# Optimization experiments

Measured on AMD Instinct MI355X. Metric: run time of the kernel, lower is better.

The kernel has to match this reference:

```python
import jax, jax.numpy as jnp
import numpy as np

B, T, D = 8, 4096, 512
MAX_SEG = 32  # max_segment_len


def setup_inputs() -> dict:
    key = jax.random.key(0)
    ks = jax.random.split(key, 8)
    s = 0.02
    return {
        "x": jax.random.normal(ks[0], (B, T, D), dtype=jnp.float32),
        "W1": jax.random.normal(ks[1], (D // 2, D), dtype=jnp.float32) * s,
        "b1": jnp.zeros((D // 2,), jnp.float32),
        "W2": jax.random.normal(ks[2], (2, D // 2), dtype=jnp.float32) * s,
        "b2": jnp.zeros((2,), jnp.float32),
        "W_ih": jax.random.normal(ks[3], (4 * D, D), dtype=jnp.float32) * s,
        "W_hh": jax.random.normal(ks[4], (4 * D, D), dtype=jnp.float32) * s,
        "b_ih": jax.random.normal(ks[5], (4 * D,), dtype=jnp.float32) * s,
        "b_hh": jax.random.normal(ks[6], (4 * D,), dtype=jnp.float32) * s,
    }


def reference(x, W1, b1, W2, b2, W_ih, W_hh, b_ih, b_hh):
    Bb, Tt, Dd = x.shape

    # boundary predictor (eval mode: dropout = identity, erf-based GELU)
    h1 = jax.nn.gelu(jnp.einsum('btd,hd->bth', x, W1) + b1, approximate=False)
    boundary_logits = jnp.einsum('bth,gh->btg', h1, W2) + b2  # [B,T,2]
    probs = jax.nn.softmax(boundary_logits, axis=-1)
    bnd = (probs[..., 1] > 0.5).astype(jnp.float32)

    # forced boundaries every MAX_SEG steps and at T-1
    forced = np.arange(MAX_SEG, Tt, MAX_SEG)
    bnd = bnd.at[:, forced].set(1.0).at[:, Tt - 1].set(1.0)
    is_b = bnd > 0.5                                     # [B,T] bool

    # a segment starts at t if t==0 or there was a boundary at t-1
    reset = jnp.concatenate([jnp.ones((Bb, 1), bool), is_b[:, :-1]], axis=1)

    # segmented LSTM scan: state resets at segment starts; hidden at a boundary
    # position t equals the LSTM final hidden over segment [start..t]
    gates_x = jnp.einsum('btd,gd->btg', x, W_ih) + b_ih + b_hh  # [B,T,4D]

    def scan_one(gx, rs):
        def step(carry, inp):
            h, c = carry
            g, r = inp
            h = jnp.where(r, 0.0, h)
            c = jnp.where(r, 0.0, c)
            g = g + W_hh @ h
            i, f, gg, o = jnp.split(g, 4)  # torch gate order i,f,g,o
            c = jax.nn.sigmoid(f) * c + jax.nn.sigmoid(i) * jnp.tanh(gg)
            h = jax.nn.sigmoid(o) * jnp.tanh(c)
            return (h, c), h
        z = jnp.zeros((Dd,), gx.dtype)
        _, hs = jax.lax.scan(step, (z, z), (gx, rs))
        return hs

    hs = jax.vmap(scan_one)(gates_x, reset)  # [B,T,D]

    # a segment is emitted at t iff boundary at t and segment length >= 2
    # (i.e. t is not itself a segment start)
    emit = is_b & ~reset                      # [B,T]
    seg_idx = jnp.cumsum(emit.astype(jnp.int32), axis=1) - 1
    dest = jnp.where(emit, seg_idx, Tt)       # non-emitted rows dumped at col T
    barr = jnp.arange(Bb)[:, None]

    padded = jnp.zeros((Bb, Tt + 1, Dd), x.dtype)
    padded = padded.at[barr, dest].set(hs)[:, :Tt]       # [B,T,D], zero padded

    bidx = jnp.full((Bb, Tt + 1), -1, jnp.int32)
    tgrid = jnp.broadcast_to(jnp.arange(Tt, dtype=jnp.int32)[None, :], (Bb, Tt))
    bidx = bidx.at[barr, dest].set(tgrid)[:, :Tt]        # [B,T], -1 padded

    # fallback when no segment was emitted: mean over time, boundary index T-1
    counts = emit.sum(axis=1)
    fb = counts == 0
    padded = padded.at[:, 0].set(jnp.where(fb[:, None], x.mean(axis=1), padded[:, 0]))
    bidx = bidx.at[:, 0].set(jnp.where(fb, Tt - 1, bidx[:, 0]))

    return padded, bidx, boundary_logits
```

## Files before the change

kernel.cpp:

```cpp
#include <hip/hip_runtime.h>
#include <math.h>

#define B 8
#define T 4096
#define D 512
#define H1 256
#define R 1024
#define BIDX_OFF ((size_t)B*T*D)
#define LOG_OFF  ((size_t)B*T*D + B*T)

typedef __attribute__((ext_vector_type(8))) short short8;
typedef __attribute__((ext_vector_type(4))) float f32x4;

__device__ inline unsigned short f2bf_hi(float f) {
  unsigned u = __float_as_uint(f);
  u += 0x7FFF + ((u >> 16) & 1);
  return (unsigned short)(u >> 16);
}
__device__ inline float bf2f(unsigned short b) {
  return __uint_as_float(((unsigned)b) << 16);
}
__device__ inline float sigm(float v) { return 1.f / (1.f + expf(-v)); }

__global__ __launch_bounds__(256) void k_prep(const float* __restrict__ x,
                                              const float* __restrict__ Wih,
                                              const float* __restrict__ Whh,
                                              const float* __restrict__ bih,
                                              const float* __restrict__ bhh,
                                              const float* __restrict__ W1,
                                              float* __restrict__ out,
                                              unsigned short* __restrict__ xhi,
                                              unsigned short* __restrict__ WhhH,
                                              unsigned short* __restrict__ WhhL,
                                              unsigned short* __restrict__ WxH,
                                              float* __restrict__ bsum,
                                              unsigned short* __restrict__ W1t0,
                                              unsigned short* __restrict__ W1t1,
                                              unsigned short* __restrict__ W1t2) {
  int gid = blockIdx.x * 256 + threadIdx.x;
  float4 z4 = make_float4(0.f, 0.f, 0.f, 0.f);
  float4* o4 = (float4*)out;
#pragma unroll
  for (int i = 0; i < 4; ++i) o4[(size_t)i * 1048576 + gid] = z4;
  {
    const float* xs = x + (size_t)gid * 16;
    unsigned short hv[16];
#pragma unroll
    for (int q = 0; q < 4; ++q) {
      float4 v = *(const float4*)(xs + q * 4);
      hv[q * 4 + 0] = f2bf_hi(v.x); hv[q * 4 + 1] = f2bf_hi(v.y);
      hv[q * 4 + 2] = f2bf_hi(v.z); hv[q * 4 + 3] = f2bf_hi(v.w);
    }
    uint4 p0, p1;
    p0.x = (unsigned)hv[0] | ((unsigned)hv[1] << 16);  p0.y = (unsigned)hv[2] | ((unsigned)hv[3] << 16);
    p0.z = (unsigned)hv[4] | ((unsigned)hv[5] << 16);  p0.w = (unsigned)hv[6] | ((unsigned)hv[7] << 16);
    p1.x = (unsigned)hv[8] | ((unsigned)hv[9] << 16);  p1.y = (unsigned)hv[10] | ((unsigned)hv[11] << 16);
    p1.z = (unsigned)hv[12] | ((unsigned)hv[13] << 16); p1.w = (unsigned)hv[14] | ((unsigned)hv[15] << 16);
    *(uint4*)(xhi + (size_t)gid * 16) = p0;
    *(uint4*)(xhi + (size_t)gid * 16 + 8) = p1;
  }
  {
    int n = gid >> 9, k = gid & 511;
    int d = n >> 2, g = n & 3;
    size_t oo = (size_t)(g * 512 + d) * 512 + k;
    float wx = Wih[oo], wh = Whh[oo];
    WxH[(size_t)n * 512 + k] = f2bf_hi(wx);
    unsigned short hh = f2bf_hi(wh);
    WhhH[(size_t)n * 512 + k] = hh;
    WhhL[(size_t)n * 512 + k] = f2bf_hi(wh - bf2f(hh));
    if (k == 0) bsum[n] = bih[g * 512 + d] + bhh[g * 512 + d];
  }
  if (gid < 16384) {
    int base = gid * 8;
    float4 a = *(const float4*)(W1 + base);
    float4 b = *(const float4*)(W1 + base + 4);
    float fv[8] = {a.x, a.y, a.z, a.w, b.x, b.y, b.z, b.w};
    unsigned short t0[8], t1[8], t2[8];
#pragma unroll
    for (int j = 0; j < 8; ++j) {
      unsigned short h0 = f2bf_hi(fv[j]);
      float r1 = fv[j] - bf2f(h0);
      unsigned short h1v = f2bf_hi(r1);
      float r2 = r1 - bf2f(h1v);
      t0[j] = h0; t1[j] = h1v; t2[j] = f2bf_hi(r2);
    }
    uint4 p0, p1, p2;
    p0.x = (unsigned)t0[0] | ((unsigned)t0[1] << 16); p0.y = (unsigned)t0[2] | ((unsigned)t0[3] << 16);
    p0.z = (unsigned)t0[4] | ((unsigned)t0[5] << 16); p0.w = (unsigned)t0[6] | ((unsigned)t0[7] << 16);
    p1.x = (unsigned)t1[0] | ((unsigned)t1[1] << 16); p1.y = (unsigned)t1[2] | ((unsigned)t1[3] << 16);
    p1.z = (unsigned)t1[4] | ((unsigned)t1[5] << 16); p1.w = (unsigned)t1[6] | ((unsigned)t1[7] << 16);
    p2.x = (unsigned)t2[0] | ((unsigned)t2[1] << 16); p2.y = (unsigned)t2[2] | ((unsigned)t2[3] << 16);
    p2.z = (unsigned)t2[4] | ((unsigned)t2[5] << 16); p2.w = (unsigned)t2[6] | ((unsigned)t2[7] << 16);
    *(uint4*)(W1t0 + base) = p0;
    *(uint4*)(W1t1 + base) = p1;
    *(uint4*)(W1t2 + base) = p2;
  }
}

__global__ __launch_bounds__(256) void k_bnd1f(const float* __restrict__ x,
                                               const unsigned short* __restrict__ T0,
                                               const unsigned short* __restrict__ T1,
                                               const unsigned short* __restrict__ T2,
                                               const float* __restrict__ b1,
                                               const float* __restrict__ W2,
                                               const float* __restrict__ b2,
                                               float* __restrict__ out,
                                               unsigned char* __restrict__ flags) {
  __shared__ unsigned short A0[64][40], A1[64][40], A2[64][40];
  __shared__ float part[2][64][2];
  __shared__ float lsm[64][2];
  int row0 = blockIdx.x * 64;
  int tid = threadIdx.x;
  int arow = tid >> 2, ak0 = (tid & 3) * 8;
  const float* xrow = x + (size_t)(row0 + arow) * 512;
  int w = tid >> 6, l = tid & 63;
  int wm = w >> 1, wn = w & 1;
  int lrow = l & 15, lk = (l >> 4) * 8;

  f32x4 acc[2][8];
#pragma unroll
  for (int i = 0; i < 2; ++i)
#pragma unroll
    for (int j = 0; j < 8; ++j) acc[i][j] = (f32x4)(0.f);

  for (int kb = 0; kb < 512; kb += 32) {
    float4 a0v = *(const float4*)(xrow + kb + ak0);
    float4 a1v = *(const float4*)(xrow + kb + ak0 + 4);
    float fv[8] = {a0v.x, a0v.y, a0v.z, a0v.w, a1v.x, a1v.y, a1v.z, a1v.w};
    unsigned short s0[8], s1[8], s2[8];
#pragma unroll
    for (int j = 0; j < 8; ++j) {
      unsigned short h0 = f2bf_hi(fv[j]);
      float r1 = fv[j] - bf2f(h0);
      unsigned short h1v = f2bf_hi(r1);
      float r2 = r1 - bf2f(h1v);
      s0[j] = h0; s1[j] = h1v; s2[j] = f2bf_hi(r2);
    }
    uint4 p;
    p.x = (unsigned)s0[0] | ((unsigned)s0[1] << 16); p.y = (unsigned)s0[2] | ((unsigned)s0[3] << 16);
    p.z = (unsigned)s0[4] | ((unsigned)s0[5] << 16); p.w = (unsigned)s0[6] | ((unsigned)s0[7] << 16);
    *(uint4*)&A0[arow][ak0] = p;
    p.x = (unsigned)s1[0] | ((unsigned)s1[1] << 16); p.y = (unsigned)s1[2] | ((unsigned)s1[3] << 16);
    p.z = (unsigned)s1[4] | ((unsigned)s1[5] << 16); p.w = (unsigned)s1[6] | ((unsigned)s1[7] << 16);
    *(uint4*)&A1[arow][ak0] = p;
    p.x = (unsigned)s2[0] | ((unsigned)s2[1] << 16); p.y = (unsigned)s2[2] | ((unsigned)s2[3] << 16);
    p.z = (unsigned)s2[4] | ((unsigned)s2[5] << 16); p.w = (unsigned)s2[6] | ((unsigned)s2[7] << 16);
    *(uint4*)&A2[arow][ak0] = p;
    __syncthreads();

    short8 a0f[2], a1f[2], a2f[2];
#pragma unroll
    for (int fi = 0; fi < 2; ++fi) {
      a0f[fi] = *(const short8*)&A0[wm * 32 + fi * 16 + lrow][lk];
      a1f[fi] = *(const short8*)&A1[wm * 32 + fi * 16 + lrow][lk];
      a2f[fi] = *(const short8*)&A2[wm * 32 + fi * 16 + lrow][lk];
    }
#pragma unroll
    for (int fj = 0; fj < 8; ++fj) {
      size_t bo = (size_t)(wn * 128 + fj * 16 + lrow) * 512 + kb + lk;
      short8 b0 = *(const short8*)(T0 + bo);
      short8 b1v = *(const short8*)(T1 + bo);
      short8 b2v = *(const short8*)(T2 + bo);
#pragma unroll
      for (int fi = 0; fi < 2; ++fi) {
        acc[fi][fj] = __builtin_amdgcn_mfma_f32_16x16x32_bf16(a0f[fi], b0, acc[fi][fj], 0, 0, 0);
        acc[fi][fj] = __builtin_amdgcn_mfma_f32_16x16x32_bf16(a0f[fi], b1v, acc[fi][fj], 0, 0, 0);
        acc[fi][fj] = __builtin_amdgcn_mfma_f32_16x16x32_bf16(a1f[fi], b0, acc[fi][fj], 0, 0, 0);
        acc[fi][fj] = __builtin_amdgcn_mfma_f32_16x16x32_bf16(a1f[fi], b1v, acc[fi][fj], 0, 0, 0);
        acc[fi][fj] = __builtin_amdgcn_mfma_f32_16x16x32_bf16(a0f[fi], b2v, acc[fi][fj], 0, 0, 0);
        acc[fi][fj] = __builtin_amdgcn_mfma_f32_16x16x32_bf16(a2f[fi], b0, acc[fi][fj], 0, 0, 0);
      }
    }
    __syncthreads();
  }

  float b1v[8], w20[8], w21[8];
#pragma unroll
  for (int fj = 0; fj < 8; ++fj) {
    int col = wn * 128 + fj * 16 + lrow;
    b1v[fj] = b1[col];
    w20[fj] = W2[col];
    w21[fj] = W2[H1 + col];
  }
  float p0[2][4], p1[2][4];
#pragma unroll
  for (int fi = 0; fi < 2; ++fi)
#pragma unroll
    for (int reg = 0; reg < 4; ++reg) { p0[fi][reg] = 0.f; p1[fi][reg] = 0.f; }
#pragma unroll
  for (int fi = 0; fi < 2; ++fi)
#pragma unroll
    for (int fj = 0; fj < 8; ++fj)
#pragma unroll
      for (int reg = 0; reg < 4; ++reg) {
        float v = acc[fi][fj][reg] + b1v[fj];
        float ge = 0.5f * v * (1.0f + erff(v * 0.70710678118654752f));
        p0[fi][reg] = fmaf(ge, w20[fj], p0[fi][reg]);
        p1[fi][reg] = fmaf(ge, w21[fj], p1[fi][reg]);
      }
#pragma unroll
  for (int off = 1; off < 16; off <<= 1)
#pragma unroll
    for (int fi = 0; fi < 2; ++fi)
#pragma unroll
      for (int reg = 0; reg < 4; ++reg) {
        p0[fi][reg] += __shfl_xor(p0[fi][reg], off);
        p1[fi][reg] += __shfl_xor(p1[fi][reg], off);
      }
  if (lrow == 0) {
    int hi = l >> 4;
#pragma unroll
    for (int fi = 0; fi < 2; ++fi)
#pragma unroll
      for (int reg = 0; reg < 4; ++reg) {
        int rloc = wm * 32 + fi * 16 + hi * 4 + reg;
        part[wn][rloc][0] = p0[fi][reg];
        part[wn][rloc][1] = p1[fi][reg];
      }
  }
  __syncthreads();
  if (tid < 128) {
    int r = tid >> 1, g = tid & 1;
    float lg = part[0][r][g] + part[1][r][g] + b2[g];
    int rowg = row0 + r;
    out[LOG_OFF + (size_t)rowg * 2 + g] = lg;
    lsm[r][g] = lg;
  }
  __syncthreads();
  if (tid < 64) {
    int rowg = row0 + tid;
    int t = rowg & (T - 1);
    bool forced = (((t & 31) == 0) && t != 0) || (t == T - 1);
    flags[rowg] = (forced || (lsm[tid][1] > lsm[tid][0])) ? 1 : 0;
  }
}

__global__ __launch_bounds__(256) void k_seg(unsigned char* __restrict__ flags,
                                             int* __restrict__ segidx,
                                             int* __restrict__ counts,
                                             float* __restrict__ out) {
  int b = blockIdx.x, tid = threadIdx.x;
  __shared__ int sc[256];
  const int PER = T / 256;
  int base = tid * PER;
  bool em[PER];
  unsigned char prev = (tid == 0) ? 0 : (unsigned char)(flags[b * T + base - 1] & 1);
  int cnt = 0;
  for (int i = 0; i < PER; ++i) {
    int t = base + i;
    unsigned char cur = flags[b * T + t] & 1;
    bool reset = (t == 0) || (prev != 0);
    bool e = (cur != 0) && !reset;
    em[i] = e;
    cnt += e ? 1 : 0;
    flags[b * T + t] = (unsigned char)(cur | (reset ? 2 : 0) | (e ? 4 : 0));
    prev = cur;
  }
  sc[tid] = cnt;
  __syncthreads();
  for (int off = 1; off < 256; off <<= 1) {
    int v = (tid >= off) ? sc[tid - off] : 0;
    __syncthreads();
    sc[tid] += v;
    __syncthreads();
  }
  int total = sc[255];
  int run = sc[tid] - cnt;
  for (int i = 0; i < PER; ++i) {
    if (em[i]) { segidx[b * T + base + i] = run; run++; }
  }
  for (int j = tid; j < T; j += 256) out[BIDX_OFF + (size_t)b * T + j] = -1.0f;
  __syncthreads();
  run = sc[tid] - cnt;
  for (int i = 0; i < PER; ++i) {
    if (em[i]) { out[BIDX_OFF + (size_t)b * T + run] = (float)(base + i); run++; }
  }
  if (tid == 0) counts[b] = total;
}

__global__ __launch_bounds__(256) void k_gx(const unsigned short* __restrict__ xhi,
                                            const unsigned short* __restrict__ WxH,
                                            unsigned short* __restrict__ gx) {
  __shared__ unsigned short As[128][40], Bs[128][40];
  __shared__ unsigned short Cs[64][136];
  int m0 = blockIdx.x * 128, n0 = blockIdx.y * 128;
  int tid = threadIdx.x;
  int row = tid >> 1, col0 = (tid & 1) * 16;
  const unsigned short* asrc = xhi + (size_t)(m0 + row) * 512 + col0;
  const unsigned short* bsrc = WxH + (size_t)(n0 + row) * 512 + col0;

  int w = tid >> 6, l = tid & 63;
  int wm = w >> 1, wn = w & 1;
  int lrow = l & 15, lk = (l >> 4) * 8;

  f32x4 acc[4][4];
#pragma unroll
  for (int i = 0; i < 4; ++i)
#pragma unroll
    for (int j = 0; j < 4; ++j) acc[i][j] = (f32x4)(0.f);

  uint4 rA0 = *(const uint4*)asrc,       rA1 = *(const uint4*)(asrc + 8);
  uint4 rB0 = *(const uint4*)bsrc,       rB1 = *(const uint4*)(bsrc + 8);

  for (int it = 0; it < 16; ++it) {
    *(uint4*)&As[row][col0] = rA0;  *(uint4*)&As[row][col0 + 8] = rA1;
    *(uint4*)&Bs[row][col0] = rB0;  *(uint4*)&Bs[row][col0 + 8] = rB1;
    __syncthreads();
    if (it < 15) {
      int ko = (it + 1) * 32;
      rA0 = *(const uint4*)(asrc + ko);  rA1 = *(const uint4*)(asrc + ko + 8);
      rB0 = *(const uint4*)(bsrc + ko);  rB1 = *(const uint4*)(bsrc + ko + 8);
    }
    short8 af[4], bf[4];
#pragma unroll
    for (int fi = 0; fi < 4; ++fi) {
      af[fi] = *(const short8*)&As[wm * 64 + fi * 16 + lrow][lk];
      bf[fi] = *(const short8*)&Bs[wn * 64 + fi * 16 + lrow][lk];
    }
#pragma unroll
    for (int fi = 0; fi < 4; ++fi)
#pragma unroll
      for (int fj = 0; fj < 4; ++fj)
        acc[fi][fj] = __builtin_amdgcn_mfma_f32_16x16x32_bf16(af[fi], bf[fj], acc[fi][fj], 0, 0, 0);
    __syncthreads();
  }

#pragma unroll
  for (int h = 0; h < 2; ++h) {
    if (wm == h) {
#pragma unroll
      for (int fi = 0; fi < 4; ++fi)
#pragma unroll
        for (int fj = 0; fj < 4; ++fj) {
          int lr = fi * 16 + (l >> 4) * 4;
          int lc = wn * 64 + fj * 16 + lrow;
#pragma unroll
          for (int reg = 0; reg < 4; ++reg)
            Cs[lr + reg][lc] = f2bf_hi(acc[fi][fj][reg]);
        }
    }
    __syncthreads();
    int crow = tid >> 2, c0 = (tid & 3) * 32;
    size_t gbase = (size_t)(m0 + h * 64 + crow) * 2048 + n0 + c0;
    *(uint4*)(gx + gbase)      = *(uint4*)&Cs[crow][c0];
    *(uint4*)(gx + gbase + 8)  = *(uint4*)&Cs[crow][c0 + 8];
    *(uint4*)(gx + gbase + 16) = *(uint4*)&Cs[crow][c0 + 16];
    *(uint4*)(gx + gbase + 24) = *(uint4*)&Cs[crow][c0 + 24];
    __syncthreads();
  }
}

__global__ __launch_bounds__(256) void k_cell0(const unsigned short* __restrict__ gx,
                                               const float* __restrict__ bsum,
                                               const unsigned char* __restrict__ flags,
                                               const int* __restrict__ segidx,
                                               unsigned short* __restrict__ Hhi,
                                               unsigned short* __restrict__ Hlo,
                                               float* __restrict__ Cb,
                                               float* __restrict__ out) {
  int id = blockIdx.x * 256 + threadIdx.x;
  int rr = id >> 9, d = id & 511;
  int ch = rr & 127, bb = rr >> 7;
  int t = ch ? (32 * ch + 1) : 0;
  uint2 gp = *(const uint2*)(gx + ((size_t)(bb * T + t) * 2048 + 4 * d));
  float4 bsv = *(const float4*)&bsum[4 * d];
  float gi_ = bf2f((unsigned short)(gp.x & 0xffff)) + bsv.x;
  float gz_ = bf2f((unsigned short)(gp.y & 0xffff)) + bsv.z;
  float go_ = bf2f((unsigned short)(gp.y >> 16)) + bsv.w;
  float c = sigm(gi_) * tanhf(gz_);
  float h = sigm(go_) * tanhf(c);
  unsigned char fl = flags[bb * T + t];
  if (fl & 4) {
    int si = segidx[bb * T + t];
    out[(size_t)(bb * T + si) * D + d] = h;
  }
  bool isb = (fl & 1) != 0;
  float he = isb ? 0.f : h;
  float ce = isb ? 0.f : c;
  Cb[(size_t)rr * D + d] = ce;
  unsigned short hh = f2bf_hi(he);
  Hhi[(size_t)rr * D + d] = hh;
  Hlo[(size_t)rr * D + d] = f2bf_hi(he - bf2f(hh));
}

__global__ __launch_bounds__(256) void k_step2(const unsigned short* __restrict__ gx,
                                               const unsigned short* __restrict__ WhhH,
                                               const unsigned short* __restrict__ WhhL,
                                               const unsigned short* __restrict__ HhR,
                                               const unsigned short* __restrict__ HlR,
                                               unsigned short* __restrict__ HhW,
                                               unsigned short* __restrict__ HlW,
                                               float* __restrict__ Cb,
                                               const float* __restrict__ bsum,
                                               const unsigned char* __restrict__ flags,
                                               const int* __restrict__ segidx,
                                               float* __restrict__ out, int s) {
  __shared__ unsigned short Ah[64][72], Al[64][72], Bh[64][72], Bl[64][72];
  __shared__ float Ct[64][68];
  int id = blockIdx.x;
  int swz = (id & 7) * 64 + (id >> 3);
  int bn = swz >> 4, bm = swz & 15;
  int tid = threadIdx.x;
  int row = tid >> 2, col0 = (tid & 3) * 16;
  int ra = bm * 64 + row;
  const unsigned short* ah_src = HhR + (size_t)ra * D;
  const unsigned short* al_src = HlR + (size_t)ra * D;
  const unsigned short* bh_src = WhhH + (size_t)(bn * 64 + row) * D;
  const unsigned short* bl_src = WhhL + (size_t)(bn * 64 + row) * D;

  int w = tid >> 6, l = tid & 63;
  int wm = w >> 1, wn = w & 1;
  int lrow = l & 15, lk = (l >> 4) * 8;

  f32x4 acc[2][2];
#pragma unroll
  for (int i = 0; i < 2; ++i)
#pragma unroll
    for (int j = 0; j < 2; ++j) acc[i][j] = (f32x4)(0.f);

  uint4 rAh0 = *(const uint4*)(ah_src + col0), rAh1 = *(const uint4*)(ah_src + col0 + 8);
  uint4 rAl0 = *(const uint4*)(al_src + col0), rAl1 = *(const uint4*)(al_src + col0 + 8);
  uint4 rBh0 = *(const uint4*)(bh_src + col0), rBh1 = *(const uint4*)(bh_src + col0 + 8);
  uint4 rBl0 = *(const uint4*)(bl_src + col0), rBl1 = *(const uint4*)(bl_src + col0 + 8);

  for (int kk = 0; kk < 8; ++kk) {
    *(uint4*)&Ah[row][col0] = rAh0;  *(uint4*)&Ah[row][col0 + 8] = rAh1;
    *(uint4*)&Al[row][col0] = rAl0;  *(uint4*)&Al[row][col0 + 8] = rAl1;
    *(uint4*)&Bh[row][col0] = rBh0;  *(uint4*)&Bh[row][col0 + 8] = rBh1;
    *(uint4*)&Bl[row][col0] = rBl0;  *(uint4*)&Bl[row][col0 + 8] = rBl1;
    __syncthreads();
    if (kk < 7) {
      int ko = (kk + 1) * 64 + col0;
      rAh0 = *(const uint4*)(ah_src + ko); rAh1 = *(const uint4*)(ah_src + ko + 8);
      rAl0 = *(const uint4*)(al_src + ko); rAl1 = *(const uint4*)(al_src + ko + 8);
      rBh0 = *(const uint4*)(bh_src + ko); rBh1 = *(const uint4*)(bh_src + ko + 8);
      rBl0 = *(const uint4*)(bl_src + ko); rBl1 = *(const uint4*)(bl_src + ko + 8);
    }
#pragma unroll
    for (int ks = 0; ks < 2; ++ks) {
      short8 ah0 = *(const short8*)&Ah[wm * 32 + lrow][ks * 32 + lk];
      short8 ah1 = *(const short8*)&Ah[wm * 32 + 16 + lrow][ks * 32 + lk];
      short8 al0 = *(const short8*)&Al[wm * 32 + lrow][ks * 32 + lk];
      short8 al1 = *(const short8*)&Al[wm * 32 + 16 + lrow][ks * 32 + lk];
      short8 bh0 = *(const short8*)&Bh[wn * 32 + lrow][ks * 32 + lk];
      short8 bh1 = *(const short8*)&Bh[wn * 32 + 16 + lrow][ks * 32 + lk];
      short8 bl0 = *(const short8*)&Bl[wn * 32 + lrow][ks * 32 + lk];
      short8 bl1 = *(const short8*)&Bl[wn * 32 + 16 + lrow][ks * 32 + lk];
      acc[0][0] = __builtin_amdgcn_mfma_f32_16x16x32_bf16(ah0, bh0, acc[0][0], 0, 0, 0);
      acc[0][1] = __builtin_amdgcn_mfma_f32_16x16x32_bf16(ah0, bh1, acc[0][1], 0, 0, 0);
      acc[1][0] = __builtin_amdgcn_mfma_f32_16x16x32_bf16(ah1, bh0, acc[1][0], 0, 0, 0);
      acc[1][1] = __builtin_amdgcn_mfma_f32_16x16x32_bf16(ah1, bh1, acc[1][1], 0, 0, 0);
      acc[0][0] = __builtin_amdgcn_mfma_f32_16x16x32_bf16(ah0, bl0, acc[0][0], 0, 0, 0);
      acc[0][1] = __builtin_amdgcn_mfma_f32_16x16x32_bf16(ah0, bl1, acc[0][1], 0, 0, 0);
      acc[1][0] = __builtin_amdgcn_mfma_f32_16x16x32_bf16(ah1, bl0, acc[1][0], 0, 0, 0);
      acc[1][1] = __builtin_amdgcn_mfma_f32_16x16x32_bf16(ah1, bl1, acc[1][1], 0, 0, 0);
      acc[0][0] = __builtin_amdgcn_mfma_f32_16x16x32_bf16(al0, bh0, acc[0][0], 0, 0, 0);
      acc[0][1] = __builtin_amdgcn_mfma_f32_16x16x32_bf16(al0, bh1, acc[0][1], 0, 0, 0);
      acc[1][0] = __builtin_amdgcn_mfma_f32_16x16x32_bf16(al1, bh0, acc[1][0], 0, 0, 0);
      acc[1][1] = __builtin_amdgcn_mfma_f32_16x16x32_bf16(al1, bh1, acc[1][1], 0, 0, 0);
    }
    __syncthreads();
  }

#pragma unroll
  for (int fi = 0; fi < 2; ++fi)
#pragma unroll
    for (int fj = 0; fj < 2; ++fj) {
      int crow = wm * 32 + fi * 16 + (l >> 4) * 4;
      int ccol = wn * 32 + fj * 16 + lrow;
#pragma unroll
      for (int reg = 0; reg < 4; ++reg)
        Ct[crow + reg][ccol] = acc[fi][fj][reg];
    }
  __syncthreads();

  int d_loc = tid & 15, rb = tid >> 4;
  int d_g = bn * 16 + d_loc;
  float4 bsv = *(const float4*)&bsum[(size_t)4 * d_g];
#pragma unroll
  for (int j = 0; j < 4; ++j) {
    int r_loc = rb + 16 * j;
    int r = bm * 64 + r_loc;
    int ch = r & 127, bb = r >> 7;
    int len = (ch == 0) ? 33 : ((ch == 127) ? 31 : 32);
    if (s >= len) continue;
    int t = (ch ? (32 * ch + 1) : 0) + s;
    unsigned char fl = flags[bb * T + t];
    float4 g = *(float4*)&Ct[r_loc][4 * d_loc];
    uint2 gp = *(const uint2*)(gx + ((size_t)(bb * T + t) * 2048 + 4 * d_g));
    float gi = g.x + bsv.x + bf2f((unsigned short)(gp.x & 0xffff));
    float gf = g.y + bsv.y + bf2f((unsigned short)(gp.x >> 16));
    float gz = g.z + bsv.z + bf2f((unsigned short)(gp.y & 0xffff));
    float go = g.w + bsv.w + bf2f((unsigned short)(gp.y >> 16));
    float cp = Cb[(size_t)r * D + d_g];
    float c = sigm(gf) * cp + sigm(gi) * tanhf(gz);
    float h = sigm(go) * tanhf(c);
    if (fl & 4) {
      int si = segidx[bb * T + t];
      out[(size_t)(bb * T + si) * D + d_g] = h;
    }
    bool isb = (fl & 1) != 0;
    float he = isb ? 0.f : h;
    float ce = isb ? 0.f : c;
    Cb[(size_t)r * D + d_g] = ce;
    unsigned short hh = f2bf_hi(he);
    HhW[(size_t)r * D + d_g] = hh;
    HlW[(size_t)r * D + d_g] = f2bf_hi(he - bf2f(hh));
  }
}

__global__ __launch_bounds__(256) void k_tail(const unsigned short* __restrict__ gx,
                                              const unsigned short* __restrict__ WhhH,
                                              const unsigned short* __restrict__ WhhL,
                                              const unsigned short* __restrict__ Hhi,
                                              const unsigned short* __restrict__ Hlo,
                                              const float* __restrict__ Cb,
                                              const float* __restrict__ bsum,
                                              const unsigned char* __restrict__ flags,
                                              const int* __restrict__ segidx,
                                              float* __restrict__ out) {
  __shared__ float hsh[512];
  __shared__ float gsh[128][4];
  int bb = blockIdx.x >> 2, q = blockIdx.x & 3;
  int r = bb * 128;
  int tid = threadIdx.x;
  for (int i = tid; i < 512; i += 256)
    hsh[i] = bf2f(Hhi[(size_t)r * 512 + i]) + bf2f(Hlo[(size_t)r * 512 + i]);
  __syncthreads();
  int dd_loc = tid >> 1;
  int dd = q * 128 + dd_loc;
  int pair = tid & 1;
#pragma unroll
  for (int gg = 0; gg < 2; ++gg) {
    int n = 4 * dd + 2 * pair + gg;
    const unsigned short* wh = WhhH + (size_t)n * 512;
    const unsigned short* wl = WhhL + (size_t)n * 512;
    float sacc = 0.f;
    for (int k = 0; k < 512; k += 8) {
      uint4 ph = *(const uint4*)(wh + k);
      uint4 pl = *(const uint4*)(wl + k);
      unsigned pu[4] = {ph.x, ph.y, ph.z, ph.w};
      unsigned lu[4] = {pl.x, pl.y, pl.z, pl.w};
#pragma unroll
      for (int j = 0; j < 4; ++j) {
        float w0 = bf2f((unsigned short)(pu[j] & 0xffff)) + bf2f((unsigned short)(lu[j] & 0xffff));
        float w1 = bf2f((unsigned short)(pu[j] >> 16)) + bf2f((unsigned short)(lu[j] >> 16));
        sacc = fmaf(w0, hsh[k + 2 * j], sacc);
        sacc = fmaf(w1, hsh[k + 2 * j + 1], sacc);
      }
    }
    unsigned short gxv = gx[(size_t)(bb * T + 32) * 2048 + n];
    gsh[dd_loc][2 * pair + gg] = sacc + bf2f(gxv) + bsum[n];
  }
  __syncthreads();
  if (pair == 0) {
    unsigned char fl = flags[bb * T + 32];
    float gi = gsh[dd_loc][0], gf = gsh[dd_loc][1], gz = gsh[dd_loc][2], go = gsh[dd_loc][3];
    float cp = Cb[(size_t)r * 512 + dd];
    float c = sigm(gf) * cp + sigm(gi) * tanhf(gz);
    float h = sigm(go) * tanhf(c);
    if (fl & 4) {
      int si = segidx[bb * T + 32];
      out[(size_t)(bb * T + si) * D + dd] = h;
    }
  }
}

__global__ __launch_bounds__(256) void k_fb(const float* __restrict__ x,
                                            const int* __restrict__ counts,
                                            float* __restrict__ out) {
  int b = blockIdx.x;
  if (counts[b] != 0) return;
  int tid = threadIdx.x;
  for (int d = tid; d < D; d += 256) {
    float sum = 0.f;
    for (int t = 0; t < T; ++t) sum += x[(size_t)(b * T + t) * D + d];
    out[(size_t)(b * T) * D + d] = sum / (float)T;
  }
  if (tid == 0) out[BIDX_OFF + (size_t)b * T] = (float)(T - 1);
}


extern "C" void kernel_launch(void* const* d_in, const int* in_sizes, int n_in,
                              void* d_out, int out_size, void* d_ws, size_t ws_size,
                              hipStream_t stream) {
  const float* x   = (const float*)d_in[0];
  const float* W1  = (const float*)d_in[1];
  const float* b1  = (const float*)d_in[2];
  const float* W2  = (const float*)d_in[3];
  const float* b2  = (const float*)d_in[4];
  const float* Wih = (const float*)d_in[5];
  const float* Whh = (const float*)d_in[6];
  const float* bih = (const float*)d_in[7];
  const float* bhh = (const float*)d_in[8];
  float* out = (float*)d_out;
  char* ws = (char*)d_ws;
  const size_t MB = 1 << 20;

  unsigned char* flags = (unsigned char*)(ws + 0);
  int* counts = (int*)(ws + 32768);
  int* segidx = (int*)(ws + 65536);
  unsigned short* Hh0  = (unsigned short*)(ws + 1 * MB);
  unsigned short* Hl0  = (unsigned short*)(ws + 2 * MB);
  unsigned short* Hh1  = (unsigned short*)(ws + 3 * MB);
  unsigned short* Hl1  = (unsigned short*)(ws + 4 * MB);
  float* Cb            = (float*)(ws + 5 * MB);
  unsigned short* WhhH = (unsigned short*)(ws + 7 * MB);
  unsigned short* WhhL = (unsigned short*)(ws + 9 * MB);
  unsigned short* WxH  = (unsigned short*)(ws + 11 * MB);
  float* bsum          = (float*)(ws + 13 * MB);
  unsigned short* W1t0 = (unsigned short*)(ws + 13 * MB + 262144);
  unsigned short* W1t1 = (unsigned short*)(ws + 13 * MB + 2 * 262144);
  unsigned short* W1t2 = (unsigned short*)(ws + 13 * MB + 3 * 262144);
  unsigned short* xhi  = (unsigned short*)(ws + 14 * MB);
  unsigned short* gx   = (unsigned short*)(ws + 46 * MB);

  hipLaunchKernelGGL(k_prep, dim3(4096), dim3(256), 0, stream,
                     x, Wih, Whh, bih, bhh, W1, out, xhi, WhhH, WhhL, WxH,
                     bsum, W1t0, W1t1, W1t2);
  hipLaunchKernelGGL(k_bnd1f, dim3(512), dim3(256), 0, stream,
                     x, W1t0, W1t1, W1t2, b1, W2, b2, out, flags);
  hipLaunchKernelGGL(k_seg, dim3(8), dim3(256), 0, stream, flags, segidx, counts, out);
  hipLaunchKernelGGL(k_gx, dim3(256, 16), dim3(256), 0, stream, xhi, WxH, gx);
  hipLaunchKernelGGL(k_cell0, dim3(2048), dim3(256), 0, stream, gx, bsum, flags, segidx, Hh0, Hl0, Cb, out);
  for (int s = 1; s < 32; ++s) {
    const unsigned short* HhR = ((s - 1) & 1) ? Hh1 : Hh0;
    const unsigned short* HlR = ((s - 1) & 1) ? Hl1 : Hl0;
    unsigned short* HhW = (s & 1) ? Hh1 : Hh0;
    unsigned short* HlW = (s & 1) ? Hl1 : Hl0;
    hipLaunchKernelGGL(k_step2, dim3(512), dim3(256), 0, stream,
                       gx, WhhH, WhhL, HhR, HlR, HhW, HlW, Cb, bsum, flags, segidx, out, s);
  }
  hipLaunchKernelGGL(k_tail, dim3(32), dim3(256), 0, stream,
                     gx, WhhH, WhhL, Hh1, Hl1, Cb, bsum, flags, segidx, out);
  hipLaunchKernelGGL(k_fb, dim3(8), dim3(256), 0, stream, x, counts, out);
}
```

Measured before the change: 848.0 us.

## Split boundary MLP into tiled GEMM with LDS-staged weights plus logit kernel

```diff
diff --git a/kernel.cpp b/kernel.cpp
--- a/kernel.cpp
+++ b/kernel.cpp
@@ -97,31 +97,29 @@
   }
 }
 
-__global__ __launch_bounds__(256) void k_bnd1f(const float* __restrict__ x,
-                                               const unsigned short* __restrict__ T0,
-                                               const unsigned short* __restrict__ T1,
-                                               const unsigned short* __restrict__ T2,
-                                               const float* __restrict__ b1,
-                                               const float* __restrict__ W2,
-                                               const float* __restrict__ b2,
-                                               float* __restrict__ out,
-                                               unsigned char* __restrict__ flags) {
-  __shared__ unsigned short A0[64][40], A1[64][40], A2[64][40];
-  __shared__ float part[2][64][2];
-  __shared__ float lsm[64][2];
-  int row0 = blockIdx.x * 64;
+__global__ __launch_bounds__(256) void k_bnd1(const float* __restrict__ x,
+                                              const unsigned short* __restrict__ T0,
+                                              const unsigned short* __restrict__ T1,
+                                              const unsigned short* __restrict__ T2,
+                                              const float* __restrict__ b1,
+                                              float* __restrict__ h1out) {
+  __shared__ unsigned short A0[64][48], A1[64][48], A2[64][48];
+  __shared__ unsigned short B0[64][48], B1[64][48], B2[64][48];
+  int bm = blockIdx.x, bnn = blockIdx.y;
   int tid = threadIdx.x;
   int arow = tid >> 2, ak0 = (tid & 3) * 8;
-  const float* xrow = x + (size_t)(row0 + arow) * 512;
+  const float* xrow = x + (size_t)(bm * 64 + arow) * 512;
+  size_t wro = (size_t)(bnn * 64 + arow) * 512;
+
   int w = tid >> 6, l = tid & 63;
   int wm = w >> 1, wn = w & 1;
   int lrow = l & 15, lk = (l >> 4) * 8;
 
-  f32x4 acc[2][8];
+  f32x4 acc[2][2];
 #pragma unroll
   for (int i = 0; i < 2; ++i)
 #pragma unroll
-    for (int j = 0; j < 8; ++j) acc[i][j] = (f32x4)(0.f);
+    for (int j = 0; j < 2; ++j) acc[i][j] = (f32x4)(0.f);
 
   for (int kb = 0; kb < 512; kb += 32) {
     float4 a0v = *(const float4*)(xrow + kb + ak0);
@@ -146,92 +144,83 @@
     p.x = (unsigned)s2[0] | ((unsigned)s2[1] << 16); p.y = (unsigned)s2[2] | ((unsigned)s2[3] << 16);
     p.z = (unsigned)s2[4] | ((unsigned)s2[5] << 16); p.w = (unsigned)s2[6] | ((unsigned)s2[7] << 16);
     *(uint4*)&A2[arow][ak0] = p;
-    __syncthreads();
-
-    short8 a0f[2], a1f[2], a2f[2];
+
+    *(uint4*)&B0[arow][ak0] = *(const uint4*)(T0 + wro + kb + ak0);
+    *(uint4*)&B1[arow][ak0] = *(const uint4*)(T1 + wro + kb + ak0);
+    *(uint4*)&B2[arow][ak0] = *(const uint4*)(T2 + wro + kb + ak0);
+    __syncthreads();
+
+    short8 a0f[2], a1f[2], a2f[2], b0f[2], b1f[2], b2f[2];
 #pragma unroll
     for (int fi = 0; fi < 2; ++fi) {
       a0f[fi] = *(const short8*)&A0[wm * 32 + fi * 16 + lrow][lk];
       a1f[fi] = *(const short8*)&A1[wm * 32 + fi * 16 + lrow][lk];
       a2f[fi] = *(const short8*)&A2[wm * 32 + fi * 16 + lrow][lk];
-    }
-#pragma unroll
-    for (int fj = 0; fj < 8; ++fj) {
-      size_t bo = (size_t)(wn * 128 + fj * 16 + lrow) * 512 + kb + lk;
-      short8 b0 = *(const short8*)(T0 + bo);
-      short8 b1v = *(const short8*)(T1 + bo);
-      short8 b2v = *(const short8*)(T2 + bo);
-#pragma unroll
-      for (int fi = 0; fi < 2; ++fi) {
-        acc[fi][fj] = __builtin_amdgcn_mfma_f32_16x16x32_bf16(a0f[fi], b0, acc[fi][fj], 0, 0, 0);
-        acc[fi][fj] = __builtin_amdgcn_mfma_f32_16x16x32_bf16(a0f[fi], b1v, acc[fi][fj], 0, 0, 0);
-        acc[fi][fj] = __builtin_amdgcn_mfma_f32_16x16x32_bf16(a1f[fi], b0, acc[fi][fj], 0, 0, 0);
-        acc[fi][fj] = __builtin_amdgcn_mfma_f32_16x16x32_bf16(a1f[fi], b1v, acc[fi][fj], 0, 0, 0);
-        acc[fi][fj] = __builtin_amdgcn_mfma_f32_16x16x32_bf16(a0f[fi], b2v, acc[fi][fj], 0, 0, 0);
-        acc[fi][fj] = __builtin_amdgcn_mfma_f32_16x16x32_bf16(a2f[fi], b0, acc[fi][fj], 0, 0, 0);
+      b0f[fi] = *(const short8*)&B0[wn * 32 + fi * 16 + lrow][lk];
+      b1f[fi] = *(const short8*)&B1[wn * 32 + fi * 16 + lrow][lk];
+      b2f[fi] = *(const short8*)&B2[wn * 32 + fi * 16 + lrow][lk];
+    }
+#pragma unroll
+    for (int fi = 0; fi < 2; ++fi)
+#pragma unroll
+      for (int fj = 0; fj < 2; ++fj) {
+        acc[fi][fj] = __builtin_amdgcn_mfma_f32_16x16x32_bf16(a0f[fi], b0f[fj], acc[fi][fj], 0, 0, 0);
+        acc[fi][fj] = __builtin_amdgcn_mfma_f32_16x16x32_bf16(a0f[fi], b1f[fj], acc[fi][fj], 0, 0, 0);
+        acc[fi][fj] = __builtin_amdgcn_mfma_f32_16x16x32_bf16(a1f[fi], b0f[fj], acc[fi][fj], 0, 0, 0);
+        acc[fi][fj] = __builtin_amdgcn_mfma_f32_16x16x32_bf16(a1f[fi], b1f[fj], acc[fi][fj], 0, 0, 0);
+        acc[fi][fj] = __builtin_amdgcn_mfma_f32_16x16x32_bf16(a0f[fi], b2f[fj], acc[fi][fj], 0, 0, 0);
+        acc[fi][fj] = __builtin_amdgcn_mfma_f32_16x16x32_bf16(a2f[fi], b0f[fj], acc[fi][fj], 0, 0, 0);
       }
-    }
-    __syncthreads();
-  }
-
-  float b1v[8], w20[8], w21[8];
-#pragma unroll
-  for (int fj = 0; fj < 8; ++fj) {
-    int col = wn * 128 + fj * 16 + lrow;
-    b1v[fj] = b1[col];
-    w20[fj] = W2[col];
-    w21[fj] = W2[H1 + col];
-  }
-  float p0[2][4], p1[2][4];
+    __syncthreads();
+  }
 #pragma unroll
   for (int fi = 0; fi < 2; ++fi)
 #pragma unroll
-    for (int reg = 0; reg < 4; ++reg) { p0[fi][reg] = 0.f; p1[fi][reg] = 0.f; }
-#pragma unroll
-  for (int fi = 0; fi < 2; ++fi)
-#pragma unroll
-    for (int fj = 0; fj < 8; ++fj)
+    for (int fj = 0; fj < 2; ++fj) {
+      int rrow = bm * 64 + wm * 32 + fi * 16 + (l >> 4) * 4;
+      int rcol = bnn * 64 + wn * 32 + fj * 16 + lrow;
+      float bv = b1[rcol];
 #pragma unroll
       for (int reg = 0; reg < 4; ++reg) {
-        float v = acc[fi][fj][reg] + b1v[fj];
+        float v = acc[fi][fj][reg] + bv;
         float ge = 0.5f * v * (1.0f + erff(v * 0.70710678118654752f));
-        p0[fi][reg] = fmaf(ge, w20[fj], p0[fi][reg]);
-        p1[fi][reg] = fmaf(ge, w21[fj], p1[fi][reg]);
+        h1out[(size_t)(rrow + reg) * H1 + rcol] = ge;
       }
-#pragma unroll
-  for (int off = 1; off < 16; off <<= 1)
-#pragma unroll
-    for (int fi = 0; fi < 2; ++fi)
-#pragma unroll
-      for (int reg = 0; reg < 4; ++reg) {
-        p0[fi][reg] += __shfl_xor(p0[fi][reg], off);
-        p1[fi][reg] += __shfl_xor(p1[fi][reg], off);
-      }
-  if (lrow == 0) {
-    int hi = l >> 4;
-#pragma unroll
-    for (int fi = 0; fi < 2; ++fi)
-#pragma unroll
-      for (int reg = 0; reg < 4; ++reg) {
-        int rloc = wm * 32 + fi * 16 + hi * 4 + reg;
-        part[wn][rloc][0] = p0[fi][reg];
-        part[wn][rloc][1] = p1[fi][reg];
-      }
-  }
-  __syncthreads();
-  if (tid < 128) {
-    int r = tid >> 1, g = tid & 1;
-    float lg = part[0][r][g] + part[1][r][g] + b2[g];
-    int rowg = row0 + r;
-    out[LOG_OFF + (size_t)rowg * 2 + g] = lg;
-    lsm[r][g] = lg;
-  }
-  __syncthreads();
-  if (tid < 64) {
-    int rowg = row0 + tid;
-    int t = rowg & (T - 1);
+    }
+}
+
+__global__ __launch_bounds__(256) void k_log(const float* __restrict__ h1,
+                                             const float* __restrict__ W2,
+                                             const float* __restrict__ b2,
+                                             float* __restrict__ out,
+                                             unsigned char* __restrict__ flags) {
+  int tid = threadIdx.x;
+  int row = blockIdx.x * 32 + (tid >> 3);
+  int part = tid & 7;
+  const float* hr = h1 + (size_t)row * H1 + part * 32;
+  const float* w0 = W2 + part * 32;
+  const float* w1 = W2 + H1 + part * 32;
+  float s0 = 0.f, s1 = 0.f;
+#pragma unroll
+  for (int q = 0; q < 8; ++q) {
+    float4 hv = *(const float4*)(hr + q * 4);
+    float4 w0v = *(const float4*)(w0 + q * 4);
+    float4 w1v = *(const float4*)(w1 + q * 4);
+    s0 = fmaf(hv.x, w0v.x, fmaf(hv.y, w0v.y, fmaf(hv.z, w0v.z, fmaf(hv.w, w0v.w, s0))));
+    s1 = fmaf(hv.x, w1v.x, fmaf(hv.y, w1v.y, fmaf(hv.z, w1v.z, fmaf(hv.w, w1v.w, s1))));
+  }
+#pragma unroll
+  for (int off = 4; off >= 1; off >>= 1) {
+    s0 += __shfl_xor(s0, off);
+    s1 += __shfl_xor(s1, off);
+  }
+  if (part == 0) {
+    float l0 = s0 + b2[0], l1 = s1 + b2[1];
+    out[LOG_OFF + (size_t)row * 2]     = l0;
+    out[LOG_OFF + (size_t)row * 2 + 1] = l1;
+    int t = row & (T - 1);
     bool forced = (((t & 31) == 0) && t != 0) || (t == T - 1);
-    flags[rowg] = (forced || (lsm[tid][1] > lsm[tid][0])) ? 1 : 0;
+    flags[row] = (forced || (l1 > l0)) ? 1 : 0;
   }
 }
 
@@ -398,8 +387,8 @@
   __shared__ unsigned short Ah[64][72], Al[64][72], Bh[64][72], Bl[64][72];
   __shared__ float Ct[64][68];
   int id = blockIdx.x;
-  int swz = (id & 7) * 64 + (id >> 3);
-  int bn = swz >> 4, bm = swz & 15;
+  int bm = (id & 7) * 2 + (id >> 8);
+  int bn = (id >> 3) & 31;
   int tid = threadIdx.x;
   int row = tid >> 2, col0 = (tid & 3) * 16;
   int ra = bm * 64 + row;
@@ -614,12 +603,13 @@
   unsigned short* W1t2 = (unsigned short*)(ws + 13 * MB + 3 * 262144);
   unsigned short* xhi  = (unsigned short*)(ws + 14 * MB);
   unsigned short* gx   = (unsigned short*)(ws + 46 * MB);
+  float* h1buf         = (float*)(ws + 46 * MB);
 
   hipLaunchKernelGGL(k_prep, dim3(4096), dim3(256), 0, stream,
                      x, Wih, Whh, bih, bhh, W1, out, xhi, WhhH, WhhL, WxH,
                      bsum, W1t0, W1t1, W1t2);
-  hipLaunchKernelGGL(k_bnd1f, dim3(512), dim3(256), 0, stream,
-                     x, W1t0, W1t1, W1t2, b1, W2, b2, out, flags);
+  hipLaunchKernelGGL(k_bnd1, dim3(512, 4), dim3(256), 0, stream, x, W1t0, W1t1, W1t2, b1, h1buf);
+  hipLaunchKernelGGL(k_log, dim3(1024), dim3(256), 0, stream, h1buf, W2, b2, out, flags);
   hipLaunchKernelGGL(k_seg, dim3(8), dim3(256), 0, stream, flags, segidx, counts, out);
   hipLaunchKernelGGL(k_gx, dim3(256, 16), dim3(256), 0, stream, xhi, WxH, gx);
   hipLaunchKernelGGL(k_cell0, dim3(2048), dim3(256), 0, stream, gx, bsum, flags, segidx, Hh0, Hl0, Cb, out);
```

Result: faster. 771.7 us (-9.0%).
